# Kernel optimization log

Measured on AMD Instinct MI355X. Metric: run time of the kernel, lower is better.

The kernel has to match this reference:

```python
import jax, jax.numpy as jnp
import numpy as np

EPS = 1e-5  # BatchNorm eps (torch default)

def _wq(w):
    # W8A16 fake-quant: per-output-channel symmetric int8 quantize + dequantize
    s = jnp.max(jnp.abs(w), axis=tuple(range(1, w.ndim)), keepdims=True) / 127.0
    s = jnp.maximum(s, 1e-8)
    q = jnp.clip(jnp.round(w / s), -128.0, 127.0)
    return q * s

def _conv(x, w, b, pad):
    y = jax.lax.conv_general_dilated(x, _wq(w), (1, 1), [(pad, pad), (pad, pad)],
                                     dimension_numbers=('NCHW', 'OIHW', 'NCHW'))
    return y + b[None, :, None, None]

def _bn(x, g, b, m, v):
    sh = (1, -1, 1, 1) if x.ndim == 4 else (1, -1)
    inv = jax.lax.rsqrt(v + EPS)
    return (x - m.reshape(sh)) * (inv * g).reshape(sh) + b.reshape(sh)

def _pool(x):
    return jax.lax.reduce_window(x, -jnp.inf, jax.lax.max, (1, 1, 2, 2), (1, 1, 2, 2), 'VALID')

def _ht(x):
    return jnp.clip(x, -1.0, 1.0)

def _linear(x, w, b):
    return x @ _wq(w).T + b

def setup_inputs() -> dict:
    key = jax.random.key(0)
    ks = iter(jax.random.split(key, 64))
    def rn(shape, s=0.05):
        return jax.random.normal(next(ks), shape, jnp.float32) * s
    d = {}
    d['x'] = jax.random.normal(next(ks), (1024, 1, 28, 28), jnp.float32)
    convs = [(1, 32, 5), (32, 64, 5), (64, 128, 3), (128, 256, 3), (256, 256, 1)]
    for i, (ci, co, k) in enumerate(convs, 1):
        d[f'w{i}'] = rn((co, ci, k, k), 0.1)
        d[f'b{i}'] = rn((co,))
        d[f'g{i}'] = jnp.ones((co,), jnp.float32)
        d[f'be{i}'] = jnp.zeros((co,), jnp.float32)
        d[f'mu{i}'] = rn((co,))
        d[f'va{i}'] = jax.random.uniform(next(ks), (co,), jnp.float32, 0.5, 1.5)
    fcs = [(2304, 1024), (1024, 512)]
    for i, (fi, fo) in enumerate(fcs, 1):
        d[f'fw{i}'] = rn((fo, fi), 0.05)
        d[f'fb{i}'] = rn((fo,))
        d[f'fg{i}'] = jnp.ones((fo,), jnp.float32)
        d[f'fbe{i}'] = jnp.zeros((fo,), jnp.float32)
        d[f'fmu{i}'] = rn((fo,))
        d[f'fva{i}'] = jax.random.uniform(next(ks), (fo,), jnp.float32, 0.5, 1.5)
    d['fw3'] = rn((10, 512), 0.05)
    d['fb3'] = rn((10,))
    return d

def reference(x, w1, b1, g1, be1, mu1, va1, w2, b2, g2, be2, mu2, va2,
              w3, b3, g3, be3, mu3, va3, w4, b4, g4, be4, mu4, va4,
              w5, b5, g5, be5, mu5, va5,
              fw1, fb1, fg1, fbe1, fmu1, fva1,
              fw2, fb2, fg2, fbe2, fmu2, fva2, fw3, fb3):
    h = _ht(_bn(_conv(x, w1, b1, 2), g1, be1, mu1, va1))                 # [B,32,28,28]
    h = _ht(_bn(_pool(_conv(h, w2, b2, 2)), g2, be2, mu2, va2))          # [B,64,14,14]
    h = _ht(_bn(_pool(_conv(h, w3, b3, 1)), g3, be3, mu3, va3))          # [B,128,7,7]
    h = _ht(_bn(_pool(_conv(h, w4, b4, 1)), g4, be4, mu4, va4))          # [B,256,3,3]
    h = _ht(_bn(_conv(h, w5, b5, 0), g5, be5, mu5, va5))                 # [B,256,3,3]
    h = h.reshape(h.shape[0], -1)                                        # [B,2304]
    h = _ht(_bn(_linear(h, fw1, fb1), fg1, fbe1, fmu1, fva1))            # [B,1024]
    h = _ht(_bn(_linear(h, fw2, fb2), fg2, fbe2, fmu2, fva2))            # [B,512]
    return _linear(h, fw3, fb3)                                          # [B,10]
```

## Files before the change

### kernel.cpp

```cpp
#include <hip/hip_runtime.h>
#include <hip/hip_bf16.h>
#include <math.h>


#define EPS 1e-5f

typedef __attribute__((ext_vector_type(8))) short bf16x8;
typedef __attribute__((ext_vector_type(4))) float f32x4;
typedef __attribute__((ext_vector_type(16))) float f32x16;
typedef __attribute__((ext_vector_type(4))) int i32x4;

__device__ __forceinline__ short f2bf(float f) {
  unsigned u = __builtin_bit_cast(unsigned, f);
  unsigned r = u + 0x7FFFu + ((u >> 16) & 1u);
  return (short)(r >> 16);
}
__device__ __forceinline__ float bf2f(short h) {
  unsigned u = ((unsigned)(unsigned short)h) << 16;
  return __builtin_bit_cast(float, u);
}
__device__ __forceinline__ int swz(int pin, int smask) {
  return (pin ^ (pin >> 2)) & smask;
}
__device__ __forceinline__ float qclip(float w, float s) {
  return fminf(fmaxf(rintf(w / s), -128.f), 127.f);
}

struct PrepArgs {
  const float* w[8];
  short* dsth[8];
  float* dstf;
  float* sc;
  int sco[8];
  int cik[8];
  int kind[8];
  int KK[8];
  int CI[8];
  int OCCH[8];
  int KC[8];
  int cum[9];
};

__global__ __launch_bounds__(256) void prep_all(PrepArgs a) {
  int b = blockIdx.x;
  int t = 0;
  while (b >= a.cum[t + 1]) t++;
  int oc = b - a.cum[t];
  int cik = a.cik[t];
  const float* src = a.w[t] + (size_t)oc * cik;
  float m = 0.f;
  for (int i = threadIdx.x; i < cik; i += 256) m = fmaxf(m, fabsf(src[i]));
  #pragma unroll
  for (int o = 1; o < 64; o <<= 1) m = fmaxf(m, __shfl_xor(m, o));
  __shared__ float red[4];
  __shared__ float ssh;
  if ((threadIdx.x & 63) == 0) red[threadIdx.x >> 6] = m;
  __syncthreads();
  if (threadIdx.x == 0) {
    m = fmaxf(fmaxf(red[0], red[1]), fmaxf(red[2], red[3]));
    float s = fmaxf(m / 127.0f, 1e-8f);
    ssh = s;
    a.sc[a.sco[t] + oc] = s;
  }
  __syncthreads();
  const float s = ssh;
  const int kind = a.kind[t];
  short* dst = a.dsth[t];
  if (kind == 0) {
    for (int tt = threadIdx.x; tt < 32; tt += 256) {
      float q = (tt < 25) ? qclip(src[tt], s) : 0.f;
      dst[(((oc >> 4) * 4 + (tt >> 3)) * 16 + (oc & 15)) * 8 + (tt & 7)] = f2bf(q);
    }
  } else if (kind == 1) {
    const int KK = a.KK[t], CI = a.CI[t], OCCH = a.OCCH[t];
    const int NT32 = OCCH >> 5, KS16 = CI >> 4;
    const int chunk = oc / OCCH, ocl = oc - chunk * OCCH;
    const int nt = ocl >> 5, n32 = ocl & 31;
    for (int idx = threadIdx.x; idx < cik; idx += 256) {
      int ci = idx / KK, kk = idx - ci * KK;
      float q = qclip(src[idx], s);
      int ks = ci >> 4, hh = (ci >> 3) & 1, j = ci & 7;
      size_t d = ((((size_t)(chunk * KK + kk) * NT32 + nt) * KS16 + ks) * 64 +
                  hh * 32 + n32) * 8 + j;
      dst[d] = f2bf(q);
    }
  } else if (kind == 2) {
    const int KK = a.KK[t], CI = a.CI[t], OCCH = a.OCCH[t];
    const int NTC = OCCH >> 4, KS = CI >> 5;
    const int chunk = oc / OCCH, ocl = oc - chunk * OCCH;
    const int ntl = ocl >> 4, mr = ocl & 15;
    for (int idx = threadIdx.x; idx < cik; idx += 256) {
      int ci = idx / KK, kk = idx - ci * KK;
      float q = qclip(src[idx], s);
      int ks = ci >> 5, qq = (ci >> 3) & 3, j = ci & 7;
      size_t d = ((((((size_t)(chunk * KK + kk) * NTC + ntl) * KS + ks) * 4 + qq) *
                   16 + mr)) * 8 + j;
      dst[d] = f2bf(q);
    }
  } else if (kind == 3) {
    const int KC = a.KC[t];
    const int nblk = oc >> 6, ntl = (oc >> 4) & 3, mr = oc & 15;
    for (int k = threadIdx.x; k < cik; k += 256) {
      float q = qclip(src[k], s);
      size_t d = ((((((size_t)nblk * KC + (k >> 7)) * 4 + ntl) * 4 + ((k >> 5) & 3)) *
                   4 + ((k >> 3) & 3)) * 16 + mr) * 8 + (k & 7);
      dst[d] = f2bf(q);
    }
  } else {
    for (int k = threadIdx.x; k < cik; k += 256)
      a.dstf[(size_t)oc * cik + k] = qclip(src[k], s) * s;
  }
}

struct BnArgs {
  const float* p[7][5];
  const float* wsc;
  float* ab;
  int C[7];
  int abo[7];
  int sco[7];
  int cum[8];
};

__global__ __launch_bounds__(256) void bn_all(BnArgs a) {
  int i = blockIdx.x * 256 + threadIdx.x;
  if (i >= a.cum[7]) return;
  int t = 0;
  while (i >= a.cum[t + 1]) t++;
  int c = i - a.cum[t];
  float A = a.p[t][1][c] / sqrtf(a.p[t][4][c] + EPS);
  float B = (a.p[t][0][c] - a.p[t][3][c]) * A + a.p[t][2][c];
  a.ab[a.abo[t] + c] = A * a.wsc[a.sco[t] + c];
  a.ab[a.abo[t] + a.C[t] + c] = B;
}

__global__ __launch_bounds__(448, 2) void conv1_mfma(
    const float* __restrict__ x, const short* __restrict__ wb1,
    const float* __restrict__ ab, short* __restrict__ out) {
  __shared__ __align__(16) float sx[784];
  __shared__ __align__(16) short sim[784 * 32];
  __shared__ __align__(16) short sw1[1024];
  const int tid = threadIdx.x;
  const int img = blockIdx.x;
  for (int i = tid; i < 784; i += 448) sx[i] = x[(size_t)img * 784 + i];
  for (int i = tid; i < 1024; i += 448) sw1[i] = wb1[i];
  __syncthreads();
  for (int i = tid; i < 25088; i += 448) {
    int p = i >> 5, t = i & 31;
    short v = 0;
    if (t < 25) {
      int py = p / 28, px = p - py * 28;
      int iy = py + t / 5 - 2, ix = px + t % 5 - 2;
      if ((unsigned)iy < 28u && (unsigned)ix < 28u) v = f2bf(sx[iy * 28 + ix]);
    }
    sim[i] = v;
  }
  __syncthreads();
  const int lane = tid & 63, wv = tid >> 6;
  const int mrow = lane & 15, quad = lane >> 4;
  f32x4 acc[7][2];
  #pragma unroll
  for (int i = 0; i < 7; ++i) {
    acc[i][0] = (f32x4){0.f, 0.f, 0.f, 0.f};
    acc[i][1] = (f32x4){0.f, 0.f, 0.f, 0.f};
  }
  #pragma unroll
  for (int i = 0; i < 7; ++i) {
    const int mt = wv * 7 + i;
    const bf16x8 a = *(const bf16x8*)&sim[(mt * 16 + mrow) * 32 + quad * 8];
    #pragma unroll
    for (int nt = 0; nt < 2; ++nt) {
      const bf16x8 b = *(const bf16x8*)&sw1[(nt * 4 + quad) * 128 + mrow * 8];
      acc[i][nt] = __builtin_amdgcn_mfma_f32_16x16x32_bf16(a, b, acc[i][nt], 0, 0, 0);
    }
  }
  #pragma unroll
  for (int i = 0; i < 7; ++i) {
    const int mt = wv * 7 + i;
    #pragma unroll
    for (int nt = 0; nt < 2; ++nt) {
      const int oc = nt * 16 + mrow;
      const float A = ab[oc], Bc = ab[32 + oc];
      #pragma unroll
      for (int r = 0; r < 4; ++r) {
        const int p = mt * 16 + quad * 4 + r;
        float v = fminf(fmaxf(acc[i][nt][r] * A + Bc, -1.f), 1.f);
        out[((size_t)img * 784 + p) * 32 + oc] = f2bf(v);
      }
    }
  }
}

__global__ __launch_bounds__(256, 2) void conv2_half(
    const short* __restrict__ in, const short* __restrict__ wfrag,
    const float* __restrict__ ab, short* __restrict__ out) {
  constexpr int S = 4;
  __shared__ __align__(16) short simg[18 * 28 * 32];
  __shared__ __align__(16) short sw[5 * 2048];
  __shared__ __align__(16) short zfrag[8];
  const int tid = threadIdx.x;
  const int img = blockIdx.x >> 1, half = blockIdx.x & 1;
  const int lane = tid & 63, wv = tid >> 6;
  const int l31 = lane & 31, h = lane >> 5;
  if (tid < 8) zfrag[tid] = 0;

  {
    const i32x4* gin = (const i32x4*)(in + ((size_t)img * 784 + half * 12 * 28) * 32);
    const int lyb = half ? 0 : 2;
    for (int c = tid; c < 1792; c += 256) {
      int ps = c >> 2, blk = c & 3;
      int pin_l = (lyb + ps / 28) * 28 + ps % 28;
      ((i32x4*)simg)[pin_l * S + (blk ^ swz(pin_l, 3))] = gin[c];
    }
  }

  int ygl[4], yll[4], xx[4], ppb[4];
  bool uv[4], rv[4];
  #pragma unroll
  for (int i = 0; i < 4; ++i) {
    int u = wv + i * 4;
    uv[i] = u < 13;
    int m = u * 32 + l31;
    int ppl = m >> 2, cd = m & 3;
    rv[i] = uv[i] && (ppl < 98);
    int pr = ppl / 14, pc = ppl - pr * 14;
    ygl[i] = (half * 7 + pr) * 2 + (cd >> 1);
    yll[i] = ygl[i] - (half * 14 - 2);
    xx[i] = pc * 2 + (cd & 1);
    ppb[i] = u * 8;
  }

  f32x16 acc[4][2];
  #pragma unroll
  for (int i = 0; i < 4; ++i)
    #pragma unroll
    for (int nt = 0; nt < 2; ++nt)
      #pragma unroll
      for (int e = 0; e < 16; ++e) acc[i][nt][e] = 0.f;

  for (int tg = 0; tg < 5; ++tg) {
    __syncthreads();
    const i32x4* wsrc = (const i32x4*)(wfrag + tg * 5 * 2048);
    for (int u2 = tid; u2 < 1280; u2 += 256) ((i32x4*)sw)[u2] = wsrc[u2];
    __syncthreads();
    #pragma unroll
    for (int tt = 0; tt < 5; ++tt) {
      const int t = tg * 5 + tt;
      const int dy = t / 5 - 2, dx = t % 5 - 2;
      int aoff[4], sxh[4];
      #pragma unroll
      for (int i = 0; i < 4; ++i) {
        int iy = ygl[i] + dy, ix = xx[i] + dx;
        bool ok = rv[i] && ((unsigned)iy < 28u) && ((unsigned)ix < 28u);
        int pin_l = (yll[i] + dy) * 28 + ix;
        aoff[i] = ok ? pin_l * (S * 8) : -1;
        sxh[i] = swz(pin_l, 3);
      }
      #pragma unroll
      for (int ks = 0; ks < 2; ++ks) {
        bf16x8 af[4];
        #pragma unroll
        for (int i = 0; i < 4; ++i) {
          const short* p = (aoff[i] >= 0)
              ? &simg[aoff[i] + (((ks * 2 + h) ^ sxh[i]) * 8)] : zfrag;
          af[i] = *(const bf16x8*)p;
        }
        #pragma unroll
        for (int nt = 0; nt < 2; ++nt) {
          const bf16x8 bf = *(const bf16x8*)&sw[(((tt * 2 + nt) * 2 + ks) * 64 + lane) * 8];
          #pragma unroll
          for (int i = 0; i < 4; ++i)
            acc[i][nt] = __builtin_amdgcn_mfma_f32_32x32x16_bf16(af[i], bf, acc[i][nt], 0, 0, 0);
        }
      }
    }
  }

  #pragma unroll
  for (int i = 0; i < 4; ++i) {
    #pragma unroll
    for (int nt = 0; nt < 2; ++nt) {
      const int oc = nt * 32 + l31;
      const float A = ab[oc], Bc = ab[64 + oc];
      #pragma unroll
      for (int g = 0; g < 4; ++g) {
        const int ppo = ppb[i] + 2 * g + h;
        if (uv[i] && ppo < 98) {
          float mx = fmaxf(fmaxf(acc[i][nt][g * 4 + 0], acc[i][nt][g * 4 + 1]),
                           fmaxf(acc[i][nt][g * 4 + 2], acc[i][nt][g * 4 + 3]));
          float v = fminf(fmaxf(mx * A + Bc, -1.f), 1.f);
          out[((size_t)img * 196 + half * 98 + ppo) * 64 + oc] = f2bf(v);
        }
      }
    }
  }
}

template <int CIN, int COUT, int KW, int PAD, int IN_W, int PW, int IMGS,
          int TPI, int MTW, int OCCH, int TG, int WAVES>
__global__ __launch_bounds__(256, 2) void conv23_mfma32(
    const short* __restrict__ in, const short* __restrict__ wfrag,
    const float* __restrict__ ab, short* __restrict__ out) {
  constexpr int S = CIN / 8;
  constexpr int KS16 = CIN / 16;
  constexpr int NT32 = OCCH / 32;
  constexpr int NPIX = IN_W * IN_W;
  constexpr int PP = PW * PW;
  constexpr int KK = KW * KW;
  constexpr int CHUNKS = COUT / OCCH;
  constexpr int NGRP = KK / TG;
  constexpr int WG = TG * NT32 * KS16 * 512;
  constexpr int ITEMS = IMGS * TPI;
  constexpr int INCH = IMGS * NPIX * S;

  __shared__ __align__(16) short simg[IMGS * NPIX * CIN];
  __shared__ __align__(16) short sw[WG];
  __shared__ __align__(16) short zfrag[8];

  const int tid = threadIdx.x;
  const int img0 = blockIdx.x * IMGS;
  const int lane = tid & 63, wv = tid >> 6;
  const int l31 = lane & 31, h = lane >> 5;

  if (tid < 8) zfrag[tid] = 0;

  int yy[MTW], xx[MTW], ibs[MTW], lt_[MTW], il_[MTW];
  bool rv[MTW], uv[MTW];
  #pragma unroll
  for (int i = 0; i < MTW; ++i) {
    int u = wv + i * WAVES;
    uv[i] = u < ITEMS;
    int uu = uv[i] ? u : 0;
    int il = uu / TPI, lt = uu - il * TPI;
    int m = lt * 32 + l31;
    int pp = m >> 2, cd = m & 3;
    rv[i] = uv[i] && (pp < PP);
    int py = pp / PW, px = pp - py * PW;
    yy[i] = py * 2 + (cd >> 1);
    xx[i] = px * 2 + (cd & 1);
    ibs[i] = il * (NPIX * S);
    lt_[i] = lt; il_[i] = il;
  }

  {
    const i32x4* gsrc = (const i32x4*)(in + (size_t)img0 * NPIX * CIN);
    for (int c = tid; c < INCH; c += 256) {
      int il = c / (NPIX * S);
      int r = c - il * (NPIX * S);
      int pix = r / S;
      int blk = r & (S - 1);
      ((i32x4*)simg)[il * (NPIX * S) + pix * S + (blk ^ swz(pix, S - 1))] = gsrc[c];
    }
  }

  for (int ch = 0; ch < CHUNKS; ++ch) {
    f32x16 acc[MTW][NT32];
    #pragma unroll
    for (int i = 0; i < MTW; ++i)
      #pragma unroll
      for (int nt = 0; nt < NT32; ++nt)
        #pragma unroll
        for (int e = 0; e < 16; ++e) acc[i][nt][e] = 0.f;

    for (int tg = 0; tg < NGRP; ++tg) {
      __syncthreads();
      const i32x4* wsrc = (const i32x4*)(wfrag +
          ((size_t)ch * KK + tg * TG) * (NT32 * KS16 * 512));
      for (int u2 = tid; u2 < WG / 8; u2 += 256) ((i32x4*)sw)[u2] = wsrc[u2];
      __syncthreads();

      #pragma unroll
      for (int tt = 0; tt < TG; ++tt) {
        const int t = tg * TG + tt;
        const int dy = t / KW - PAD, dx = t % KW - PAD;
        int aoff[MTW], sxh[MTW];
        #pragma unroll
        for (int i = 0; i < MTW; ++i) {
          int iy = yy[i] + dy, ix = xx[i] + dx;
          bool ok = rv[i] && ((unsigned)iy < (unsigned)IN_W) &&
                    ((unsigned)ix < (unsigned)IN_W);
          int pin = iy * IN_W + ix;
          aoff[i] = ok ? (ibs[i] + pin * S) * 8 : -1;
          sxh[i] = swz(pin, S - 1);
        }
        #pragma unroll
        for (int ks = 0; ks < KS16; ++ks) {
          bf16x8 af[MTW];
          #pragma unroll
          for (int i = 0; i < MTW; ++i) {
            const short* p = (aoff[i] >= 0)
                ? &simg[aoff[i] + (((ks * 2 + h) ^ sxh[i]) * 8)] : zfrag;
            af[i] = *(const bf16x8*)p;
          }
          #pragma unroll
          for (int nt = 0; nt < NT32; ++nt) {
            const bf16x8 bf = *(const bf16x8*)&sw[
                (((tt * NT32 + nt) * KS16 + ks) * 64 + lane) * 8];
            #pragma unroll
            for (int i = 0; i < MTW; ++i)
              acc[i][nt] = __builtin_amdgcn_mfma_f32_32x32x16_bf16(
                  af[i], bf, acc[i][nt], 0, 0, 0);
          }
        }
      }
    }

    #pragma unroll
    for (int i = 0; i < MTW; ++i) {
      #pragma unroll
      for (int nt = 0; nt < NT32; ++nt) {
        const int oc = ch * OCCH + nt * 32 + l31;
        const float A = ab[oc], Bc = ab[COUT + oc];
        #pragma unroll
        for (int g = 0; g < 4; ++g) {
          const int ppo = lt_[i] * 8 + 2 * g + h;
          if (uv[i] && ppo < PP) {
            float mx = fmaxf(fmaxf(acc[i][nt][g * 4 + 0], acc[i][nt][g * 4 + 1]),
                             fmaxf(acc[i][nt][g * 4 + 2], acc[i][nt][g * 4 + 3]));
            float v = fminf(fmaxf(mx * A + Bc, -1.f), 1.f);
            out[((size_t)(img0 + il_[i]) * PP + ppo) * COUT + oc] = f2bf(v);
          }
        }
      }
    }
  }
}

__global__ __launch_bounds__(512, 2) void conv4_mfma(
    const short* __restrict__ in,
    const short* __restrict__ wfrag,
    const float* __restrict__ ab,
    short* __restrict__ outH, short* __restrict__ outL) {
  constexpr int S = 16, NPIX = 49, PP = 9;
  __shared__ __align__(16) short simg[2 * NPIX * 128];
  __shared__ __align__(16) short swb[2][32768];
  const int tid = threadIdx.x;
  const int img0 = blockIdx.x * 2;
  const int lane = tid & 63, wv = tid >> 6;
  const int mrow = lane & 15, quad = lane >> 4;

  {
    const i32x4* gsrc = (const i32x4*)(in + (size_t)img0 * NPIX * 128);
    for (int c = tid; c < 2 * NPIX * S; c += 512) {
      int il = c / (NPIX * S);
      int r = c - il * (NPIX * S);
      int pix = r >> 4, blk = r & 15;
      ((i32x4*)simg)[il * NPIX * S + pix * S + (blk ^ (pix & 15))] = gsrc[c];
    }
    for (int u = tid; u < 4096; u += 512)
      ((i32x4*)swb[0])[u] = ((const i32x4*)wfrag)[u];
  }

  int yy[6], xx[6], ibs[6], ppo_[6], ilv[6];
  bool rv[6], pv[6];
  #pragma unroll
  for (int i = 0; i < 6; ++i) {
    int il = i / 3, lt = i - il * 3;
    int m = lt * 16 + mrow;
    int pp = m >> 2, cd = m & 3;
    rv[i] = pp < PP;
    int py = pp / 3, px = pp - py * 3;
    yy[i] = py * 2 + (cd >> 1);
    xx[i] = px * 2 + (cd & 1);
    ibs[i] = il * NPIX * S;
    ilv[i] = il;
    ppo_[i] = lt * 4 + quad;
    pv[i] = ppo_[i] < PP;
  }
  const int nt0 = wv, nt1 = wv + 8;
  f32x4 acc[6][2];
  #pragma unroll
  for (int i = 0; i < 6; ++i) {
    acc[i][0] = (f32x4){0.f, 0.f, 0.f, 0.f};
    acc[i][1] = (f32x4){0.f, 0.f, 0.f, 0.f};
  }
  __syncthreads();

  int dy = -1, dx = -1;
  for (int t = 0; t < 9; ++t) {
    const int buf = t & 1;
    if (t < 8) {
      const i32x4* wsrc = (const i32x4*)(wfrag + (size_t)(t + 1) * 32768);
      for (int u = tid; u < 4096; u += 512) ((i32x4*)swb[buf ^ 1])[u] = wsrc[u];
    }
    #pragma unroll
    for (int ks = 0; ks < 4; ++ks) {
      bf16x8 af[6];
      #pragma unroll
      for (int i = 0; i < 6; ++i) {
        int iy = yy[i] + dy, ix = xx[i] + dx;
        bool ok = rv[i] && (unsigned)iy < 7u && (unsigned)ix < 7u;
        int pin = iy * 7 + ix;
        int blk = (ks * 4 + quad) ^ (pin & 15);
        af[i] = ok ? *(const bf16x8*)&simg[(ibs[i] + pin * S + blk) * 8]
                   : (bf16x8){0, 0, 0, 0, 0, 0, 0, 0};
      }
      const bf16x8 b0 = *(const bf16x8*)&swb[buf][((nt0 * 4 + ks) * 4 + quad) * 128 + mrow * 8];
      const bf16x8 b1 = *(const bf16x8*)&swb[buf][((nt1 * 4 + ks) * 4 + quad) * 128 + mrow * 8];
      #pragma unroll
      for (int i = 0; i < 6; ++i) {
        acc[i][0] = __builtin_amdgcn_mfma_f32_16x16x32_bf16(af[i], b0, acc[i][0], 0, 0, 0);
        acc[i][1] = __builtin_amdgcn_mfma_f32_16x16x32_bf16(af[i], b1, acc[i][1], 0, 0, 0);
      }
    }
    dx++;
    if (dx == 2) { dx = -1; dy++; }
    __syncthreads();
  }

  #pragma unroll
  for (int i = 0; i < 6; ++i) {
    if (pv[i]) {
      #pragma unroll
      for (int nj = 0; nj < 2; ++nj) {
        const int oc = (nj ? nt1 : nt0) * 16 + mrow;
        const f32x4 a = acc[i][nj];
        float mx = fmaxf(fmaxf(a[0], a[1]), fmaxf(a[2], a[3]));
        float v = fminf(fmaxf(mx * ab[oc] + ab[256 + oc], -1.f), 1.f);
        const int m5 = (img0 + ilv[i]) * 9 + ppo_[i];
        size_t d = ((((((size_t)(m5 >> 6) * 2 + (oc >> 7)) * 4 + ((m5 >> 4) & 3)) * 4 +
                     ((oc >> 5) & 3)) * 4 + ((oc >> 3) & 3)) * 16 + (m5 & 15)) * 8 + (oc & 7);
        short hi = f2bf(v);
        outH[d] = hi;
        outL[d] = f2bf(v - bf2f(hi));
      }
    }
  }
}

template <int KC, int OUTMODE, int KC2, int NALL>
__global__ __launch_bounds__(256, 2) void fc_mfma(
    const short* __restrict__ Xh, const short* __restrict__ Xl,
    const short* __restrict__ Wf, const float* __restrict__ ab,
    float* __restrict__ outF, short* __restrict__ outH, short* __restrict__ outL) {
  __shared__ __align__(16) short sxh[8192];
  __shared__ __align__(16) short sxl[8192];
  __shared__ __align__(16) short swt[8192];
  const int tid = threadIdx.x;
  const int bn = blockIdx.x, bm = blockIdx.y;
  const int lane = tid & 63, wv = tid >> 6;
  const int mrow = lane & 15, quad = lane >> 4;
  f32x4 acc[4];
  #pragma unroll
  for (int nt = 0; nt < 4; ++nt) acc[nt] = (f32x4){0.f, 0.f, 0.f, 0.f};
  for (int kc = 0; kc < KC; ++kc) {
    __syncthreads();
    {
      const size_t xo = ((size_t)bm * KC + kc) * 8192;
      const size_t wo = ((size_t)bn * KC + kc) * 8192;
      #pragma unroll
      for (int u = 0; u < 4; ++u) {
        ((i32x4*)sxh)[tid + u * 256] = ((const i32x4*)(Xh + xo))[tid + u * 256];
        ((i32x4*)sxl)[tid + u * 256] = ((const i32x4*)(Xl + xo))[tid + u * 256];
        ((i32x4*)swt)[tid + u * 256] = ((const i32x4*)(Wf + wo))[tid + u * 256];
      }
    }
    __syncthreads();
    #pragma unroll
    for (int ks = 0; ks < 4; ++ks) {
      const int ao = (((wv * 4 + ks) * 4 + quad) * 16 + mrow) * 8;
      const bf16x8 ah = *(const bf16x8*)&sxh[ao];
      const bf16x8 al = *(const bf16x8*)&sxl[ao];
      #pragma unroll
      for (int nt = 0; nt < 4; ++nt) {
        const bf16x8 b = *(const bf16x8*)&swt[(((nt * 4 + ks) * 4 + quad) * 16 + mrow) * 8];
        acc[nt] = __builtin_amdgcn_mfma_f32_16x16x32_bf16(ah, b, acc[nt], 0, 0, 0);
        acc[nt] = __builtin_amdgcn_mfma_f32_16x16x32_bf16(al, b, acc[nt], 0, 0, 0);
      }
    }
  }
  #pragma unroll
  for (int nt = 0; nt < 4; ++nt) {
    const int n = bn * 64 + nt * 16 + mrow;
    const float A = ab[n], Bc = ab[NALL + n];
    #pragma unroll
    for (int r = 0; r < 4; ++r) {
      const int m = bm * 64 + wv * 16 + quad * 4 + r;
      float v = fminf(fmaxf(acc[nt][r] * A + Bc, -1.f), 1.f);
      if (OUTMODE == 0) {
        size_t d = (((((((size_t)(m >> 6) * KC2 + (n >> 7)) * 4 + ((m >> 4) & 3)) * 4 +
                       ((n >> 5) & 3)) * 4 + ((n >> 3) & 3)) * 16 + (m & 15))) * 8 + (n & 7);
        short hi = f2bf(v);
        outH[d] = hi;
        outL[d] = f2bf(v - bf2f(hi));
      } else if (OUTMODE == 1) {
        outF[(size_t)m * NALL + n] = v;
      } else {
        const int imgq = m / 9, p = m - imgq * 9;
        const int k1 = n * 9 + p;
        size_t d = ((((((size_t)(imgq >> 6) * KC2 + (k1 >> 7)) * 4 + ((imgq >> 4) & 3)) * 4 +
                     ((k1 >> 5) & 3)) * 4 + ((k1 >> 3) & 3)) * 16 + (imgq & 15)) * 8 + (k1 & 7);
        short hi = f2bf(v);
        outH[d] = hi;
        outL[d] = f2bf(v - bf2f(hi));
      }
    }
  }
}

__global__ __launch_bounds__(256) void fc3_kernel(
    const float* __restrict__ X, const float* __restrict__ W,
    const float* __restrict__ bias, float* __restrict__ out) {
  __shared__ float ws[512 * 10 + 16];
  for (int li = threadIdx.x; li < 5120; li += 256) {
    int n = li / 512, k = li - n * 512;
    ws[k * 10 + n] = W[li];
  }
  __syncthreads();
  const int il = threadIdx.x >> 4, n = threadIdx.x & 15;
  const int img = blockIdx.x * 16 + il;
  if (n < 10) {
    const float* xp = X + (size_t)img * 512;
    float s = 0.f;
    for (int k = 0; k < 512; ++k) s += xp[k] * ws[k * 10 + n];
    out[img * 10 + n] = s + bias[n];
  }
}

extern "C" void kernel_launch(void* const* d_in, const int* in_sizes, int n_in,
                              void* d_out, int out_size, void* d_ws, size_t ws_size,
                              hipStream_t stream) {
  (void)in_sizes; (void)n_in; (void)out_size; (void)ws_size;
  const float* x = (const float*)d_in[0];
  float* W = (float*)d_ws;

  float* wsc  = W + 0;
  float* ab   = W + 2304;
  float* fq3  = W + 6912;
  short* wb1  = (short*)(W + 12032);
  short* wb2  = (short*)(W + 12544);
  short* wb3  = (short*)(W + 38144);
  short* wb4  = (short*)(W + 75008);
  short* wb5  = (short*)(W + 222464);
  short* fqb1 = (short*)(W + 255232);
  short* fqb2 = (short*)(W + 1434880);
  short* h1   = (short*)(W + 1697024);
  short* h2   = (short*)(W + 14542080);
  short* h3   = (short*)(W + 20964608);
  short* h4h  = (short*)(W + 24175872);
  short* h4l  = (short*)(W + 25355520);
  short* h5h  = (short*)(W + 26535168);
  short* h5l  = (short*)(W + 27714816);
  short* f1h  = (short*)(W + 28894464);
  short* f1l  = (short*)(W + 29418752);
  float* f2   = W + 29943040;

  PrepArgs pa;
  const int widx[8] = {1, 7, 13, 19, 25, 31, 37, 43};
  short* pdst[8] = {wb1, wb2, wb3, wb4, wb5, fqb1, fqb2, nullptr};
  const int sco8[8] = {0, 32, 96, 224, 480, 736, 1760, 2272};
  const int cik8[8] = {25, 800, 576, 1152, 256, 2304, 1024, 512};
  const int co8[8] = {32, 64, 128, 256, 256, 1024, 512, 10};
  const int kind8[8] = {0, 1, 1, 2, 3, 3, 3, 4};
  const int KK8[8] = {25, 25, 9, 9, 1, 1, 1, 1};
  const int CI8[8] = {1, 32, 64, 128, 256, 2304, 1024, 512};
  const int OCCH8[8] = {32, 64, 64, 256, 256, 1024, 512, 10};
  const int KC8[8] = {1, 1, 1, 1, 2, 18, 8, 1};
  int cum = 0;
  for (int i = 0; i < 8; ++i) {
    pa.w[i] = (const float*)d_in[widx[i]];
    pa.dsth[i] = pdst[i];
    pa.sco[i] = sco8[i];
    pa.cik[i] = cik8[i];
    pa.kind[i] = kind8[i];
    pa.KK[i] = KK8[i];
    pa.CI[i] = CI8[i];
    pa.OCCH[i] = OCCH8[i];
    pa.KC[i] = KC8[i];
    pa.cum[i] = cum;
    cum += co8[i];
  }
  pa.cum[8] = cum;
  pa.dstf = fq3;
  pa.sc = wsc;
  hipLaunchKernelGGL(prep_all, dim3(cum), dim3(256), 0, stream, pa);

  BnArgs ba;
  const int bbase[7] = {2, 8, 14, 20, 26, 32, 38};
  const int bc[7] = {32, 64, 128, 256, 256, 1024, 512};
  const int abo[7] = {0, 64, 192, 448, 960, 1472, 3520};
  int bcum = 0;
  for (int t = 0; t < 7; ++t) {
    for (int j = 0; j < 5; ++j) ba.p[t][j] = (const float*)d_in[bbase[t] + j];
    ba.C[t] = bc[t];
    ba.abo[t] = abo[t];
    ba.sco[t] = sco8[t];
    ba.cum[t] = bcum;
    bcum += bc[t];
  }
  ba.cum[7] = bcum;
  ba.ab = ab;
  ba.wsc = wsc;
  hipLaunchKernelGGL(bn_all, dim3((bcum + 255) / 256), dim3(256), 0, stream, ba);

  hipLaunchKernelGGL(conv1_mfma, dim3(1024), dim3(448), 0, stream,
                     x, wb1, ab + 0, h1);
  hipLaunchKernelGGL(conv2_half, dim3(2048), dim3(256), 0, stream,
                     h1, wb2, ab + 64, h2);
  hipLaunchKernelGGL((conv23_mfma32<64, 128, 3, 1, 14, 7, 2, 7, 4, 64, 3, 4>),
                     dim3(512), dim3(256), 0, stream, h2, wb3, ab + 192, h3);
  hipLaunchKernelGGL(conv4_mfma, dim3(512), dim3(512), 0, stream,
                     h3, wb4, ab + 448, h4h, h4l);
  hipLaunchKernelGGL((fc_mfma<2, 2, 18, 256>), dim3(4, 144), dim3(256), 0, stream,
                     h4h, h4l, wb5, ab + 960, nullptr, h5h, h5l);

  hipLaunchKernelGGL((fc_mfma<18, 0, 8, 1024>), dim3(16, 16), dim3(256), 0, stream,
                     h5h, h5l, fqb1, ab + 1472, nullptr, f1h, f1l);
  hipLaunchKernelGGL((fc_mfma<8, 1, 0, 512>), dim3(8, 16), dim3(256), 0, stream,
                     f1h, f1l, fqb2, ab + 3520, f2, nullptr, nullptr);
  hipLaunchKernelGGL(fc3_kernel, dim3(64), dim3(256), 0, stream,
                     f2, fq3, (const float*)d_in[44], (float*)d_out);
}
```

Baseline: 436.6 us.

## Pad conv2/conv3 shared tiles and double-buffer weight loads via registers

Conv2 and conv3 now stage the input image into shared memory with a zeroed halo, with rows padded to a power-of-two stride. This removes the per-tap bounds checks and the zero-fragment select from the inner MFMA loop. Weight groups are double-buffered: the next group is prefetched into registers during compute and written to the alternate shared buffer, which drops one barrier per group. Conv3 becomes a dedicated kernel that walks 18 steps (two 64-channel chunks of 9 taps), and the extra padded shared memory may reduce occupancy.

```diff
diff --git a/kernel.cpp b/kernel.cpp
--- a/kernel.cpp
+++ b/kernel.cpp
@@ -195,38 +195,54 @@
     const short* __restrict__ in, const short* __restrict__ wfrag,
     const float* __restrict__ ab, short* __restrict__ out) {
   constexpr int S = 4;
-  __shared__ __align__(16) short simg[18 * 28 * 32];
-  __shared__ __align__(16) short sw[5 * 2048];
-  __shared__ __align__(16) short zfrag[8];
+  constexpr int RS = 32;
+  __shared__ __align__(16) short simg[18 * 32 * 32];
+  __shared__ __align__(16) short sw[2][10240];
   const int tid = threadIdx.x;
   const int img = blockIdx.x >> 1, half = blockIdx.x & 1;
   const int lane = tid & 63, wv = tid >> 6;
   const int l31 = lane & 31, h = lane >> 5;
-  if (tid < 8) zfrag[tid] = 0;
-
+
+  {
+    const int padrow0 = half ? 16 : 0;
+    const int vrow0 = half ? 0 : 2;
+    for (int c = tid; c < 512; c += 256) {
+      int hp = c >> 2, blk = c & 3;
+      int pin;
+      if (hp < 64) {
+        pin = (padrow0 + (hp >> 5)) * RS + (hp & 31);
+      } else {
+        int r = (hp - 64) >> 2, cc = (hp - 64) & 3;
+        int col = (cc < 2) ? cc : (28 + cc);
+        pin = (vrow0 + r) * RS + col;
+      }
+      ((i32x4*)simg)[pin * S + blk] = (i32x4){0, 0, 0, 0};
+    }
+  }
   {
     const i32x4* gin = (const i32x4*)(in + ((size_t)img * 784 + half * 12 * 28) * 32);
-    const int lyb = half ? 0 : 2;
+    const int vrow0 = half ? 0 : 2;
     for (int c = tid; c < 1792; c += 256) {
       int ps = c >> 2, blk = c & 3;
-      int pin_l = (lyb + ps / 28) * 28 + ps % 28;
-      ((i32x4*)simg)[pin_l * S + (blk ^ swz(pin_l, 3))] = gin[c];
-    }
-  }
-
-  int ygl[4], yll[4], xx[4], ppb[4];
-  bool uv[4], rv[4];
+      int pin = (vrow0 + ps / 28) * RS + ps % 28 + 2;
+      ((i32x4*)simg)[pin * S + (blk ^ swz(pin, 3))] = gin[c];
+    }
+  }
+
+  int pinb[4], ppb[4];
+  bool uv2[4];
   #pragma unroll
   for (int i = 0; i < 4; ++i) {
     int u = wv + i * 4;
-    uv[i] = u < 13;
+    uv2[i] = u < 13;
     int m = u * 32 + l31;
     int ppl = m >> 2, cd = m & 3;
-    rv[i] = uv[i] && (ppl < 98);
+    bool ok = uv2[i] && (ppl < 98);
     int pr = ppl / 14, pc = ppl - pr * 14;
-    ygl[i] = (half * 7 + pr) * 2 + (cd >> 1);
-    yll[i] = ygl[i] - (half * 14 - 2);
-    xx[i] = pc * 2 + (cd & 1);
+    int ygl = (half * 7 + pr) * 2 + (cd >> 1);
+    int yll = ygl - (half * 14 - 2);
+    int xc = pc * 2 + (cd & 1) + 2;
+    pinb[i] = ok ? (yll * RS + xc) : (2 * RS + 2);
     ppb[i] = u * 8;
   }
 
@@ -237,43 +253,54 @@
     for (int nt = 0; nt < 2; ++nt)
       #pragma unroll
       for (int e = 0; e < 16; ++e) acc[i][nt][e] = 0.f;
+
+  i32x4 wreg[5];
+  {
+    const i32x4* ws0 = (const i32x4*)wfrag;
+    #pragma unroll
+    for (int u2 = 0; u2 < 5; ++u2) wreg[u2] = ws0[tid + u2 * 256];
+    #pragma unroll
+    for (int u2 = 0; u2 < 5; ++u2) ((i32x4*)sw[0])[tid + u2 * 256] = wreg[u2];
+  }
 
   for (int tg = 0; tg < 5; ++tg) {
     __syncthreads();
-    const i32x4* wsrc = (const i32x4*)(wfrag + tg * 5 * 2048);
-    for (int u2 = tid; u2 < 1280; u2 += 256) ((i32x4*)sw)[u2] = wsrc[u2];
-    __syncthreads();
+    if (tg < 4) {
+      const i32x4* ws = (const i32x4*)(wfrag + (size_t)(tg + 1) * 10240);
+      #pragma unroll
+      for (int u2 = 0; u2 < 5; ++u2) wreg[u2] = ws[tid + u2 * 256];
+    }
+    const short* swb = sw[tg & 1];
+    const int dy = tg - 2;
     #pragma unroll
     for (int tt = 0; tt < 5; ++tt) {
-      const int t = tg * 5 + tt;
-      const int dy = t / 5 - 2, dx = t % 5 - 2;
-      int aoff[4], sxh[4];
+      const int tp = dy * RS + (tt - 2);
+      int pin[4], sx4[4];
       #pragma unroll
       for (int i = 0; i < 4; ++i) {
-        int iy = ygl[i] + dy, ix = xx[i] + dx;
-        bool ok = rv[i] && ((unsigned)iy < 28u) && ((unsigned)ix < 28u);
-        int pin_l = (yll[i] + dy) * 28 + ix;
-        aoff[i] = ok ? pin_l * (S * 8) : -1;
-        sxh[i] = swz(pin_l, 3);
+        pin[i] = pinb[i] + tp;
+        sx4[i] = swz(pin[i], 3);
       }
       #pragma unroll
       for (int ks = 0; ks < 2; ++ks) {
         bf16x8 af[4];
         #pragma unroll
-        for (int i = 0; i < 4; ++i) {
-          const short* p = (aoff[i] >= 0)
-              ? &simg[aoff[i] + (((ks * 2 + h) ^ sxh[i]) * 8)] : zfrag;
-          af[i] = *(const bf16x8*)p;
-        }
+        for (int i = 0; i < 4; ++i)
+          af[i] = *(const bf16x8*)&simg[pin[i] * 32 + (((ks * 2 + h) ^ sx4[i]) * 8)];
         #pragma unroll
         for (int nt = 0; nt < 2; ++nt) {
-          const bf16x8 bf = *(const bf16x8*)&sw[(((tt * 2 + nt) * 2 + ks) * 64 + lane) * 8];
+          const bf16x8 bf = *(const bf16x8*)&swb[(((tt * 2 + nt) * 2 + ks) * 64 + lane) * 8];
           #pragma unroll
           for (int i = 0; i < 4; ++i)
             acc[i][nt] = __builtin_amdgcn_mfma_f32_32x32x16_bf16(af[i], bf, acc[i][nt], 0, 0, 0);
         }
       }
     }
+    if (tg < 4) {
+      #pragma unroll
+      for (int u2 = 0; u2 < 5; ++u2)
+        ((i32x4*)sw[(tg + 1) & 1])[tid + u2 * 256] = wreg[u2];
+    }
   }
 
   #pragma unroll
@@ -285,7 +312,7 @@
       #pragma unroll
       for (int g = 0; g < 4; ++g) {
         const int ppo = ppb[i] + 2 * g + h;
-        if (uv[i] && ppo < 98) {
+        if (uv2[i] && ppo < 98) {
           float mx = fmaxf(fmaxf(acc[i][nt][g * 4 + 0], acc[i][nt][g * 4 + 1]),
                            fmaxf(acc[i][nt][g * 4 + 2], acc[i][nt][g * 4 + 3]));
           float v = fminf(fmaxf(mx * A + Bc, -1.f), 1.f);
@@ -296,130 +323,126 @@
   }
 }
 
-template <int CIN, int COUT, int KW, int PAD, int IN_W, int PW, int IMGS,
-          int TPI, int MTW, int OCCH, int TG, int WAVES>
-__global__ __launch_bounds__(256, 2) void conv23_mfma32(
+__global__ __launch_bounds__(256, 2) void conv3_pad(
     const short* __restrict__ in, const short* __restrict__ wfrag,
     const float* __restrict__ ab, short* __restrict__ out) {
-  constexpr int S = CIN / 8;
-  constexpr int KS16 = CIN / 16;
-  constexpr int NT32 = OCCH / 32;
-  constexpr int NPIX = IN_W * IN_W;
-  constexpr int PP = PW * PW;
-  constexpr int KK = KW * KW;
-  constexpr int CHUNKS = COUT / OCCH;
-  constexpr int NGRP = KK / TG;
-  constexpr int WG = TG * NT32 * KS16 * 512;
-  constexpr int ITEMS = IMGS * TPI;
-  constexpr int INCH = IMGS * NPIX * S;
-
-  __shared__ __align__(16) short simg[IMGS * NPIX * CIN];
-  __shared__ __align__(16) short sw[WG];
-  __shared__ __align__(16) short zfrag[8];
-
+  constexpr int S = 8, RS = 16;
+  __shared__ __align__(16) short simg[2 * 256 * 64];
+  __shared__ __align__(16) short sw[2][4096];
   const int tid = threadIdx.x;
-  const int img0 = blockIdx.x * IMGS;
+  const int img0 = blockIdx.x * 2;
   const int lane = tid & 63, wv = tid >> 6;
   const int l31 = lane & 31, h = lane >> 5;
 
-  if (tid < 8) zfrag[tid] = 0;
-
-  int yy[MTW], xx[MTW], ibs[MTW], lt_[MTW], il_[MTW];
-  bool rv[MTW], uv[MTW];
-  #pragma unroll
-  for (int i = 0; i < MTW; ++i) {
-    int u = wv + i * WAVES;
-    uv[i] = u < ITEMS;
-    int uu = uv[i] ? u : 0;
-    int il = uu / TPI, lt = uu - il * TPI;
-    int m = lt * 32 + l31;
-    int pp = m >> 2, cd = m & 3;
-    rv[i] = uv[i] && (pp < PP);
-    int py = pp / PW, px = pp - py * PW;
-    yy[i] = py * 2 + (cd >> 1);
-    xx[i] = px * 2 + (cd & 1);
-    ibs[i] = il * (NPIX * S);
-    lt_[i] = lt; il_[i] = il;
-  }
-
+  for (int c = tid; c < 960; c += 256) {
+    int blk = c & 7, hp0 = c >> 3;
+    int il = hp0 >= 60 ? 1 : 0, hp = hp0 - il * 60;
+    int pin;
+    if (hp < 32) pin = (hp >> 4) * 15 * RS + (hp & 15);
+    else {
+      int r = ((hp - 32) >> 1) + 1, cc = ((hp - 32) & 1) * 15;
+      pin = r * RS + cc;
+    }
+    ((i32x4*)simg)[(il * 256 + pin) * S + blk] = (i32x4){0, 0, 0, 0};
+  }
   {
-    const i32x4* gsrc = (const i32x4*)(in + (size_t)img0 * NPIX * CIN);
-    for (int c = tid; c < INCH; c += 256) {
-      int il = c / (NPIX * S);
-      int r = c - il * (NPIX * S);
-      int pix = r / S;
-      int blk = r & (S - 1);
-      ((i32x4*)simg)[il * (NPIX * S) + pix * S + (blk ^ swz(pix, S - 1))] = gsrc[c];
-    }
-  }
-
-  for (int ch = 0; ch < CHUNKS; ++ch) {
-    f32x16 acc[MTW][NT32];
-    #pragma unroll
-    for (int i = 0; i < MTW; ++i)
-      #pragma unroll
-      for (int nt = 0; nt < NT32; ++nt)
+    const i32x4* gin = (const i32x4*)(in + (size_t)img0 * 196 * 64);
+    for (int c = tid; c < 3136; c += 256) {
+      int il = c / 1568, r = c - il * 1568;
+      int ps = r >> 3, blk = r & 7;
+      int pin = (ps / 14 + 1) * RS + ps % 14 + 1;
+      ((i32x4*)simg)[(il * 256 + pin) * S + (blk ^ swz(pin, 7))] = gin[c];
+    }
+  }
+
+  int pinb[4], ppb[4], ilv[4];
+  bool uv4[4];
+  #pragma unroll
+  for (int i = 0; i < 4; ++i) {
+    int u = wv + i * 4;
+    uv4[i] = u < 14;
+    int uu = uv4[i] ? u : 0;
+    int il = uu / 7, lt = uu - il * 7;
+    int m = lt * 32 + l31, ppl = m >> 2, cd = m & 3;
+    bool ok = uv4[i] && (ppl < 49);
+    int py = ppl / 7, px = ppl - py * 7;
+    int y = py * 2 + (cd >> 1), x = px * 2 + (cd & 1);
+    pinb[i] = (ok ? ((y + 1) * RS + x + 1) : (RS + 1)) + il * 256;
+    ilv[i] = il;
+    ppb[i] = lt * 8;
+  }
+
+  f32x16 acc[4][2];
+  #pragma unroll
+  for (int i = 0; i < 4; ++i)
+    #pragma unroll
+    for (int nt = 0; nt < 2; ++nt)
+      #pragma unroll
+      for (int e = 0; e < 16; ++e) acc[i][nt][e] = 0.f;
+
+  i32x4 wreg[2];
+  {
+    const i32x4* ws0 = (const i32x4*)wfrag;
+    wreg[0] = ws0[tid];
+    wreg[1] = ws0[tid + 256];
+    ((i32x4*)sw[0])[tid] = wreg[0];
+    ((i32x4*)sw[0])[tid + 256] = wreg[1];
+  }
+
+  for (int s = 0; s < 18; ++s) {
+    __syncthreads();
+    if (s < 17) {
+      const i32x4* ws = (const i32x4*)(wfrag + (size_t)(s + 1) * 4096);
+      wreg[0] = ws[tid];
+      wreg[1] = ws[tid + 256];
+    }
+    const short* swb = sw[s & 1];
+    const int t = s % 9;
+    const int tp = (t / 3 - 1) * RS + (t % 3 - 1);
+    int pin[4], sx4[4];
+    #pragma unroll
+    for (int i = 0; i < 4; ++i) {
+      pin[i] = pinb[i] + tp;
+      sx4[i] = swz(pin[i], 7);
+    }
+    #pragma unroll
+    for (int ks = 0; ks < 4; ++ks) {
+      bf16x8 af[4];
+      #pragma unroll
+      for (int i = 0; i < 4; ++i)
+        af[i] = *(const bf16x8*)&simg[pin[i] * 64 + (((ks * 2 + h) ^ sx4[i]) * 8)];
+      #pragma unroll
+      for (int nt = 0; nt < 2; ++nt) {
+        const bf16x8 bf = *(const bf16x8*)&swb[((nt * 4 + ks) * 64 + lane) * 8];
         #pragma unroll
-        for (int e = 0; e < 16; ++e) acc[i][nt][e] = 0.f;
-
-    for (int tg = 0; tg < NGRP; ++tg) {
-      __syncthreads();
-      const i32x4* wsrc = (const i32x4*)(wfrag +
-          ((size_t)ch * KK + tg * TG) * (NT32 * KS16 * 512));
-      for (int u2 = tid; u2 < WG / 8; u2 += 256) ((i32x4*)sw)[u2] = wsrc[u2];
-      __syncthreads();
-
-      #pragma unroll
-      for (int tt = 0; tt < TG; ++tt) {
-        const int t = tg * TG + tt;
-        const int dy = t / KW - PAD, dx = t % KW - PAD;
-        int aoff[MTW], sxh[MTW];
+        for (int i = 0; i < 4; ++i)
+          acc[i][nt] = __builtin_amdgcn_mfma_f32_32x32x16_bf16(af[i], bf, acc[i][nt], 0, 0, 0);
+      }
+    }
+    if (s < 17) {
+      ((i32x4*)sw[(s + 1) & 1])[tid] = wreg[0];
+      ((i32x4*)sw[(s + 1) & 1])[tid + 256] = wreg[1];
+    }
+    if (t == 8) {
+      const int ch = s / 9;
+      #pragma unroll
+      for (int i = 0; i < 4; ++i) {
         #pragma unroll
-        for (int i = 0; i < MTW; ++i) {
-          int iy = yy[i] + dy, ix = xx[i] + dx;
-          bool ok = rv[i] && ((unsigned)iy < (unsigned)IN_W) &&
-                    ((unsigned)ix < (unsigned)IN_W);
-          int pin = iy * IN_W + ix;
-          aoff[i] = ok ? (ibs[i] + pin * S) * 8 : -1;
-          sxh[i] = swz(pin, S - 1);
-        }
-        #pragma unroll
-        for (int ks = 0; ks < KS16; ++ks) {
-          bf16x8 af[MTW];
+        for (int nt = 0; nt < 2; ++nt) {
+          const int oc = ch * 64 + nt * 32 + l31;
+          const float A = ab[oc], Bc = ab[128 + oc];
           #pragma unroll
-          for (int i = 0; i < MTW; ++i) {
-            const short* p = (aoff[i] >= 0)
-                ? &simg[aoff[i] + (((ks * 2 + h) ^ sxh[i]) * 8)] : zfrag;
-            af[i] = *(const bf16x8*)p;
+          for (int g = 0; g < 4; ++g) {
+            const int ppo = ppb[i] + 2 * g + h;
+            if (uv4[i] && ppo < 49) {
+              float mx = fmaxf(fmaxf(acc[i][nt][g * 4 + 0], acc[i][nt][g * 4 + 1]),
+                               fmaxf(acc[i][nt][g * 4 + 2], acc[i][nt][g * 4 + 3]));
+              float v = fminf(fmaxf(mx * A + Bc, -1.f), 1.f);
+              out[((size_t)(img0 + ilv[i]) * 49 + ppo) * 128 + oc] = f2bf(v);
+            }
           }
           #pragma unroll
-          for (int nt = 0; nt < NT32; ++nt) {
-            const bf16x8 bf = *(const bf16x8*)&sw[
-                (((tt * NT32 + nt) * KS16 + ks) * 64 + lane) * 8];
-            #pragma unroll
-            for (int i = 0; i < MTW; ++i)
-              acc[i][nt] = __builtin_amdgcn_mfma_f32_32x32x16_bf16(
-                  af[i], bf, acc[i][nt], 0, 0, 0);
-          }
-        }
-      }
-    }
-
-    #pragma unroll
-    for (int i = 0; i < MTW; ++i) {
-      #pragma unroll
-      for (int nt = 0; nt < NT32; ++nt) {
-        const int oc = ch * OCCH + nt * 32 + l31;
-        const float A = ab[oc], Bc = ab[COUT + oc];
-        #pragma unroll
-        for (int g = 0; g < 4; ++g) {
-          const int ppo = lt_[i] * 8 + 2 * g + h;
-          if (uv[i] && ppo < PP) {
-            float mx = fmaxf(fmaxf(acc[i][nt][g * 4 + 0], acc[i][nt][g * 4 + 1]),
-                             fmaxf(acc[i][nt][g * 4 + 2], acc[i][nt][g * 4 + 3]));
-            float v = fminf(fmaxf(mx * A + Bc, -1.f), 1.f);
-            out[((size_t)(img0 + il_[i]) * PP + ppo) * COUT + oc] = f2bf(v);
-          }
+          for (int e = 0; e < 16; ++e) acc[i][nt][e] = 0.f;
         }
       }
     }
@@ -697,8 +720,8 @@
                      x, wb1, ab + 0, h1);
   hipLaunchKernelGGL(conv2_half, dim3(2048), dim3(256), 0, stream,
                      h1, wb2, ab + 64, h2);
-  hipLaunchKernelGGL((conv23_mfma32<64, 128, 3, 1, 14, 7, 2, 7, 4, 64, 3, 4>),
-                     dim3(512), dim3(256), 0, stream, h2, wb3, ab + 192, h3);
+  hipLaunchKernelGGL(conv3_pad, dim3(512), dim3(256), 0, stream,
+                     h2, wb3, ab + 192, h3);
   hipLaunchKernelGGL(conv4_mfma, dim3(512), dim3(512), 0, stream,
                      h3, wb4, ab + 448, h4h, h4l);
   hipLaunchKernelGGL((fc_mfma<2, 2, 18, 256>), dim3(4, 144), dim3(256), 0, stream,
```

Result: faster. 419.3 us (-4.0%).
